# Kernel optimization log

Measured on AMD Instinct MI355X. Metric: run time of the kernel, lower is better.

The kernel has to match this reference:

```python
import jax, jax.numpy as jnp
import numpy as np

NEG_RATIO = 5          # neg_sample_ratio, also k (num_nodes-1 >> ratio)
THRESH = 0.7           # hard_neg_threshold
SMOOTH = 0.1           # label_smoothing
NUM_NODES = 200_000
DIM = 128
B = 1024               # batch size, all labels == 1 (all positives)
FILL_VAL = -1.0e9


def _l2_normalize(x, eps=1e-12):
    # F.normalize(p=2, dim=-1): divide by clamped L2 norm
    n = jnp.sqrt(jnp.sum(x * x, axis=-1, keepdims=True))
    return x / jnp.maximum(n, eps)


def setup_inputs() -> dict:
    key = jax.random.key(0)
    k1, k2, k3, k4 = jax.random.split(key, 4)
    src_nodes = jax.random.randint(k1, (B,), 0, NUM_NODES)
    dst_nodes = jax.random.randint(k2, (B,), 0, NUM_NODES)
    labels = jnp.ones((B,), dtype=jnp.float32)  # all positives -> pos_mask all True
    timestamps = jax.random.uniform(k3, (B,), dtype=jnp.float32)
    memory = jax.random.normal(k4, (NUM_NODES, DIM), dtype=jnp.float32)
    return {
        "src_nodes": src_nodes,
        "dst_nodes": dst_nodes,
        "labels": labels,
        "timestamps": timestamps,
        "memory": memory,
    }


def reference(src_nodes, dst_nodes, labels, timestamps, memory):
    # --- embedding gather + L2 normalize ---
    src_emb = memory[src_nodes]                      # [B, D]
    s = _l2_normalize(src_emb).astype(jnp.float16)   # use_half_precision=True
    c = _l2_normalize(memory).astype(jnp.float16)    # [N, D]

    # --- similarity [B, N], back to fp32 ---
    sim = jnp.matmul(s, c.T).astype(jnp.float32)

    # --- mask out ground-truth dst and below-threshold sims ---
    cols = jnp.arange(NUM_NODES)
    allowed = cols[None, :] != dst_nodes[:, None]    # exclude GT positives
    valid = allowed & (sim > THRESH)
    score = jnp.where(valid, sim, FILL_VAL)

    # --- top-k hard negatives per positive ---
    k = NEG_RATIO  # min(neg_sample_ratio, num_nodes-1)
    topk_vals, topk_idx = jax.lax.top_k(score, k)    # [B, k]
    is_real = (topk_vals > FILL_VAL + 1.0).reshape(-1)  # [B*k]

    # --- fallback random negatives (fixed-shape equivalent of the torch
    #     pack-real-then-pad-random assembly; total count == B*k either way) ---
    rkey = jax.random.key(42)
    rand_dst = jax.random.randint(rkey, (B * k,), 0, NUM_NODES)
    src_rep = jnp.repeat(src_nodes, k)               # [B*k]
    rand_dst = jnp.where(rand_dst == src_rep, (rand_dst + 1) % NUM_NODES, rand_dst)

    final_src = src_rep
    final_dst = jnp.where(is_real, topk_idx.reshape(-1), rand_dst)
    neg_ts = jnp.repeat(timestamps, k)

    # --- assemble augmented batch ---
    new_src = jnp.concatenate([src_nodes, final_src])
    new_dst = jnp.concatenate([dst_nodes, final_dst])
    new_labels = jnp.concatenate([labels, jnp.zeros((B * k,), labels.dtype)])
    new_ts = jnp.concatenate([timestamps, neg_ts])

    # --- label smoothing ---
    new_labels = new_labels * (1.0 - SMOOTH) + (1.0 - new_labels) * SMOOTH

    return new_src, new_dst, new_labels, new_ts, topk_vals
```

## Files before the change

kernel.cpp:

```cpp
#include <hip/hip_runtime.h>

#define NUM_NODES 200000
#define DIM 128
#define BATCH 1024
#define K_NEG 5
#define CAP 16
#define NBLK 250
#define CPB 800
#define TCOL 32
#define NT 25
#define THRESH 0.7f
#define FILL (-1.0e9f)

typedef __attribute__((ext_vector_type(8))) short short8;
typedef __attribute__((ext_vector_type(16))) float f32x16;

__device__ __forceinline__ unsigned short f2bf(float x) {
  unsigned u = __builtin_bit_cast(unsigned, x);
  return (unsigned short)((u + 0x7fffu + ((u >> 16) & 1u)) >> 16);
}

__device__ __forceinline__ void stage16(const void* g, void* l) {
  __builtin_amdgcn_global_load_lds(
      (const __attribute__((address_space(1))) unsigned int*)g,
      (__attribute__((address_space(3))) unsigned int*)l,
      16, 0, 0);
}

__device__ __forceinline__ void tf2x32(unsigned k0, unsigned k1,
                                       unsigned x0, unsigned x1,
                                       unsigned* o0, unsigned* o1) {
  unsigned ks2 = k0 ^ k1 ^ 0x1BD11BDAu;
  unsigned v0 = x0 + k0, v1 = x1 + k1;
#define TFR(r) { v0 += v1; v1 = (v1 << r) | (v1 >> (32 - r)); v1 ^= v0; }
  TFR(13) TFR(15) TFR(26) TFR(6)   v0 += k1;  v1 += ks2 + 1u;
  TFR(17) TFR(29) TFR(16) TFR(24)  v0 += ks2; v1 += k0 + 2u;
  TFR(13) TFR(15) TFR(26) TFR(6)   v0 += k0;  v1 += k1 + 3u;
  TFR(17) TFR(29) TFR(16) TFR(24)  v0 += k1;  v1 += ks2 + 4u;
  TFR(13) TFR(15) TFR(26) TFR(6)   v0 += ks2; v1 += k0 + 5u;
#undef TFR
  *o0 = v0; *o1 = v1;
}

__device__ __forceinline__ unsigned rbits32(unsigned ka, unsigned kb, unsigned m) {
  unsigned o0, o1;
  tf2x32(ka, kb, 0u, m, &o0, &o1);
  return o0 ^ o1;
}

__global__ void prep_kernel(const float* __restrict__ memory,
                            const int* __restrict__ src_nodes,
                            unsigned short* __restrict__ s16f,
                            int* __restrict__ cand_cnt) {
  int tid = threadIdx.x;
  int gid = blockIdx.x * 256 + tid;
  if (gid < BATCH) cand_cnt[gid] = 0;
  int row = blockIdx.x * 4 + (tid >> 6);
  int L = tid & 63;
  int s = src_nodes[row];
  float2 v = ((const float2*)(memory + (size_t)s * DIM))[L];
  float ss = v.x * v.x + v.y * v.y;
#pragma unroll
  for (int off = 32; off > 0; off >>= 1) ss += __shfl_xor(ss, off);
  float inv = 1.0f / fmaxf(sqrtf(ss), 1e-12f);
  unsigned p = (unsigned)f2bf(v.x * inv) | ((unsigned)f2bf(v.y * inv) << 16);
  int ms = row >> 5, l32 = row & 31;
  int c = L >> 2;
  int ks = c >> 1, half = c & 1;
  ((unsigned*)s16f)[(((ms * 8 + ks) * 64) + half * 32 + l32) * 4 + (L & 3)] = p;
}

__global__ __launch_bounds__(512, 2) void sim_scan_kernel(
    const float* __restrict__ memory,
    const unsigned short* __restrict__ s16f,
    const int* __restrict__ dst_nodes,
    int* __restrict__ cand_cnt,
    float* __restrict__ cand_val,
    int* __restrict__ cand_idx) {
  __shared__ char rawb[2][16384];
  __shared__ unsigned short fragb[2][4096];
  __shared__ float nrmb[2][32];

  int tid = threadIdx.x;
  int wid = tid >> 6;
  int lane = tid & 63;
  int half = lane >> 5;
  int l32 = lane & 31;
  int jb0 = blockIdx.x * CPB;

  const char* mb = (const char*)memory;

#define STAGE(t, rbuf) {                                                        \
    int jn = jb0 + (t) * TCOL;                                                  \
    int u1 = tid;                                                               \
    int g1 = (u1 & 31) ^ ((u1 >> 6) & 7);                                       \
    stage16(mb + (size_t)(jn + g1) * 512 + ((u1 >> 5) << 4),                    \
            (char*)(rbuf) + (wid << 10));                                       \
    int u2 = tid + 512;                                                         \
    int g2 = (u2 & 31) ^ ((u2 >> 6) & 7);                                       \
    stage16(mb + (size_t)(jn + g2) * 512 + ((u2 >> 5) << 4),                    \
            (char*)(rbuf) + 8192 + (wid << 10));                                \
  }

  int ccol = wid * 4 + (lane & 3);
  int cseg = lane >> 2;
#define CONVERT(p, rbuf) {                                                      \
    const char* rb = (const char*)(rbuf);                                       \
    int xc = ccol ^ (cseg & 7);                                                 \
    float4 q0 = *(const float4*)(rb + (((2 * cseg) * 32 + xc) << 4));           \
    float4 q1 = *(const float4*)(rb + (((2 * cseg + 1) * 32 + xc) << 4));       \
    float ss = q0.x * q0.x + q0.y * q0.y + q0.z * q0.z + q0.w * q0.w            \
             + q1.x * q1.x + q1.y * q1.y + q1.z * q1.z + q1.w * q1.w;           \
    ss += __shfl_xor(ss, 4); ss += __shfl_xor(ss, 8);                           \
    ss += __shfl_xor(ss, 16); ss += __shfl_xor(ss, 32);                         \
    short8 f;                                                                   \
    f[0] = (short)f2bf(q0.x); f[1] = (short)f2bf(q0.y);                         \
    f[2] = (short)f2bf(q0.z); f[3] = (short)f2bf(q0.w);                         \
    f[4] = (short)f2bf(q1.x); f[5] = (short)f2bf(q1.y);                         \
    f[6] = (short)f2bf(q1.z); f[7] = (short)f2bf(q1.w);                         \
    *(short8*)((char*)fragb[p] + ((cseg * 32 + ccol) << 4)) = f;                \
    if (cseg == 0) nrmb[p][ccol] = fmaxf(sqrtf(ss), 1e-12f);                    \
  }

  STAGE(0, rawb[0]);
  const short8* __restrict__ af = (const short8*)s16f;
  short8 a[4][8];
#pragma unroll
  for (int m = 0; m < 4; ++m)
#pragma unroll
    for (int ks = 0; ks < 8; ++ks)
      a[m][ks] = af[(((wid * 4 + m) * 8) + ks) * 64 + lane];
  __syncthreads();
  CONVERT(0, rawb[0]);
  STAGE(1, rawb[1]);
  __syncthreads();

  f32x16 Z;
#pragma unroll
  for (int i = 0; i < 16; ++i) Z[i] = 0.0f;

  for (int t = 0; t < NT; ++t) {
    int par = t & 1;
    if (t + 2 < NT) STAGE(t + 2, rawb[par]);
    if (t + 1 < NT) CONVERT(par ^ 1, rawb[par ^ 1]);

    float nv = nrmb[par][l32];
    float thr = THRESH * nv;
    float invv = 1.0f / nv;
    int gj = jb0 + t * TCOL + l32;
    short8 bf[8];
#pragma unroll
    for (int ks = 0; ks < 8; ++ks)
      bf[ks] = *(const short8*)((char*)fragb[par] + (((2 * ks + half) * 32 + l32) << 4));

#pragma unroll
    for (int mp = 0; mp < 2; ++mp) {
      f32x16 accA = __builtin_amdgcn_mfma_f32_32x32x16_bf16(a[mp * 2][0], bf[0], Z, 0, 0, 0);
      f32x16 accB = __builtin_amdgcn_mfma_f32_32x32x16_bf16(a[mp * 2 + 1][0], bf[0], Z, 0, 0, 0);
#pragma unroll
      for (int ks = 1; ks < 8; ++ks) {
        accA = __builtin_amdgcn_mfma_f32_32x32x16_bf16(a[mp * 2][ks], bf[ks], accA, 0, 0, 0);
        accB = __builtin_amdgcn_mfma_f32_32x32x16_bf16(a[mp * 2 + 1][ks], bf[ks], accB, 0, 0, 0);
      }
      float mA = accA[0], mB = accB[0];
#pragma unroll
      for (int i = 1; i < 16; ++i) { mA = fmaxf(mA, accA[i]); mB = fmaxf(mB, accB[i]); }
      if (mA > thr || mB > thr) {
#pragma unroll
        for (int e = 0; e < 2; ++e) {
#pragma unroll
          for (int r = 0; r < 16; ++r) {
            float raw = (e == 0) ? accA[r] : accB[r];
            if (raw > thr) {
              int gi = (wid * 4 + mp * 2 + e) * 32 + (r & 3) + 8 * (r >> 2) + 4 * half;
              if (gj != dst_nodes[gi]) {
                int pq = atomicAdd(&cand_cnt[gi], 1);
                if (pq < CAP) {
                  cand_val[gi * CAP + pq] = raw * invv;
                  cand_idx[gi * CAP + pq] = gj;
                }
              }
            }
          }
        }
      }
    }

    __syncthreads();
  }
#undef STAGE
#undef CONVERT
}

__global__ void finalize_kernel(const int* __restrict__ src_nodes,
                                const int* __restrict__ dst_nodes,
                                const float* __restrict__ labels,
                                const float* __restrict__ ts,
                                const int* __restrict__ cand_cnt,
                                const float* __restrict__ cand_val,
                                const int* __restrict__ cand_idx,
                                float* __restrict__ out) {
  int r = blockIdx.x * 256 + threadIdx.x;
  if (r >= BATCH) return;
  const int TOT = BATCH + BATCH * K_NEG;
  int srcv = src_nodes[r];
  float tsv = ts[r];
  out[r] = (float)srcv;
  out[TOT + r] = (float)dst_nodes[r];
  float l = labels[r];
  out[2 * TOT + r] = l * 0.9f + (1.0f - l) * 0.1f;
  out[3 * TOT + r] = tsv;

  int cnt = cand_cnt[r];
  cnt = cnt < CAP ? cnt : CAP;
  float cv[CAP]; int ci[CAP];
  for (int i = 0; i < cnt; ++i) { cv[i] = cand_val[r * CAP + i]; ci[i] = cand_idx[r * CAP + i]; }

  unsigned k1a, k1b, k2a, k2b;
  tf2x32(0u, 42u, 0u, 0u, &k1a, &k1b);
  tf2x32(0u, 42u, 0u, 1u, &k2a, &k2b);

  const unsigned span = 200000u;
  const unsigned mult = 167296u;

  for (int s = 0; s < K_NEG; ++s) {
    int sel = -1;
    for (int i = 0; i < cnt; ++i)
      if (sel < 0 || cv[i] > cv[sel] || (cv[i] == cv[sel] && ci[i] < ci[sel])) sel = i;
    float v = FILL; int idx = 0;
    if (sel >= 0) { v = cv[sel]; idx = ci[sel]; cv[sel] = FILL; ci[sel] = 0x7fffffff; }
    bool is_real = v > (FILL + 1.0f);

    unsigned m = (unsigned)(r * K_NEG + s);
    unsigned hi = rbits32(k1a, k1b, m);
    unsigned lo = rbits32(k2a, k2b, m);
    unsigned off = ((hi % span) * mult + (lo % span)) % span;
    int rd = (int)off;
    if (rd == srcv) rd = (rd + 1) % NUM_NODES;
    int fd = is_real ? idx : rd;

    int mi = (int)m;
    out[BATCH + mi] = (float)srcv;
    out[TOT + BATCH + mi] = (float)fd;
    out[2 * TOT + BATCH + mi] = 0.1f;
    out[3 * TOT + BATCH + mi] = tsv;
    out[4 * TOT + mi] = v;
  }
}

extern "C" void kernel_launch(void* const* d_in, const int* in_sizes, int n_in,
                              void* d_out, int out_size, void* d_ws, size_t ws_size,
                              hipStream_t stream) {
  const int* src = (const int*)d_in[0];
  const int* dst = (const int*)d_in[1];
  const float* labels = (const float*)d_in[2];
  const float* ts = (const float*)d_in[3];
  const float* memory = (const float*)d_in[4];
  float* out = (float*)d_out;

  char* ws = (char*)d_ws;
  unsigned short* s16f = (unsigned short*)ws;
  int* cand_cnt = (int*)(ws + 262144);
  float* cand_val = (float*)(ws + 266240);
  int* cand_idx = (int*)(ws + 331776);

  prep_kernel<<<256, 256, 0, stream>>>(memory, src, s16f, cand_cnt);
  sim_scan_kernel<<<NBLK, 512, 0, stream>>>(memory, s16f, dst, cand_cnt, cand_val, cand_idx);
  finalize_kernel<<<(BATCH + 255) / 256, 256, 0, stream>>>(src, dst, labels, ts,
                                                           cand_cnt, cand_val, cand_idx, out);
}
```

Before: 206.0 us.

## Load memory rows directly into registers instead of staging through LDS

Replaces the global_load_lds staging of raw fp32 memory tiles, which used a double-buffered 32KB LDS region, with direct per-thread float4 register loads. Each load is issued before the MFMA work of the current tile and converted to bf16 fragments after it, so the register-held data serves as the prefetch buffer. This removes LDS traffic and frees LDS, which may help occupancy. In exchange the pipeline is one tile deep instead of two, and the extra live registers could increase register pressure.

```diff
diff --git a/kernel.cpp b/kernel.cpp
--- a/kernel.cpp
+++ b/kernel.cpp
@@ -18,13 +18,6 @@
 __device__ __forceinline__ unsigned short f2bf(float x) {
   unsigned u = __builtin_bit_cast(unsigned, x);
   return (unsigned short)((u + 0x7fffu + ((u >> 16) & 1u)) >> 16);
-}
-
-__device__ __forceinline__ void stage16(const void* g, void* l) {
-  __builtin_amdgcn_global_load_lds(
-      (const __attribute__((address_space(1))) unsigned int*)g,
-      (__attribute__((address_space(3))) unsigned int*)l,
-      16, 0, 0);
 }
 
 __device__ __forceinline__ void tf2x32(unsigned k0, unsigned k1,
@@ -77,7 +70,6 @@
     int* __restrict__ cand_cnt,
     float* __restrict__ cand_val,
     int* __restrict__ cand_idx) {
-  __shared__ char rawb[2][16384];
   __shared__ unsigned short fragb[2][4096];
   __shared__ float nrmb[2][32];
 
@@ -88,27 +80,10 @@
   int l32 = lane & 31;
   int jb0 = blockIdx.x * CPB;
 
-  const char* mb = (const char*)memory;
-
-#define STAGE(t, rbuf) {                                                        \
-    int jn = jb0 + (t) * TCOL;                                                  \
-    int u1 = tid;                                                               \
-    int g1 = (u1 & 31) ^ ((u1 >> 6) & 7);                                       \
-    stage16(mb + (size_t)(jn + g1) * 512 + ((u1 >> 5) << 4),                    \
-            (char*)(rbuf) + (wid << 10));                                       \
-    int u2 = tid + 512;                                                         \
-    int g2 = (u2 & 31) ^ ((u2 >> 6) & 7);                                       \
-    stage16(mb + (size_t)(jn + g2) * 512 + ((u2 >> 5) << 4),                    \
-            (char*)(rbuf) + 8192 + (wid << 10));                                \
-  }
-
   int ccol = wid * 4 + (lane & 3);
   int cseg = lane >> 2;
-#define CONVERT(p, rbuf) {                                                      \
-    const char* rb = (const char*)(rbuf);                                       \
-    int xc = ccol ^ (cseg & 7);                                                 \
-    float4 q0 = *(const float4*)(rb + (((2 * cseg) * 32 + xc) << 4));           \
-    float4 q1 = *(const float4*)(rb + (((2 * cseg + 1) * 32 + xc) << 4));       \
+
+#define CONVERT(p, q0, q1) {                                                    \
     float ss = q0.x * q0.x + q0.y * q0.y + q0.z * q0.z + q0.w * q0.w            \
              + q1.x * q1.x + q1.y * q1.y + q1.z * q1.z + q1.w * q1.w;           \
     ss += __shfl_xor(ss, 4); ss += __shfl_xor(ss, 8);                           \
@@ -122,7 +97,12 @@
     if (cseg == 0) nrmb[p][ccol] = fmaxf(sqrtf(ss), 1e-12f);                    \
   }
 
-  STAGE(0, rawb[0]);
+  float4 q0, q1;
+  {
+    const float4* rp4 = (const float4*)(memory + (size_t)(jb0 + ccol) * DIM);
+    q0 = rp4[cseg * 2];
+    q1 = rp4[cseg * 2 + 1];
+  }
   const short8* __restrict__ af = (const short8*)s16f;
   short8 a[4][8];
 #pragma unroll
@@ -130,9 +110,7 @@
 #pragma unroll
     for (int ks = 0; ks < 8; ++ks)
       a[m][ks] = af[(((wid * 4 + m) * 8) + ks) * 64 + lane];
-  __syncthreads();
-  CONVERT(0, rawb[0]);
-  STAGE(1, rawb[1]);
+  CONVERT(0, q0, q1);
   __syncthreads();
 
   f32x16 Z;
@@ -141,8 +119,13 @@
 
   for (int t = 0; t < NT; ++t) {
     int par = t & 1;
-    if (t + 2 < NT) STAGE(t + 2, rawb[par]);
-    if (t + 1 < NT) CONVERT(par ^ 1, rawb[par ^ 1]);
+
+    if (t + 1 < NT) {
+      const float4* rp4 =
+          (const float4*)(memory + (size_t)(jb0 + (t + 1) * TCOL + ccol) * DIM);
+      q0 = rp4[cseg * 2];
+      q1 = rp4[cseg * 2 + 1];
+    }
 
     float nv = nrmb[par][l32];
     float thr = THRESH * nv;
@@ -186,9 +169,10 @@
       }
     }
 
+    if (t + 1 < NT) CONVERT(par ^ 1, q0, q1);
+
     __syncthreads();
   }
-#undef STAGE
 #undef CONVERT
 }
 
```

New measurement: 188.3 us. 8.6% less time.
